# Kernel tuning notes

Hardware: AMD Instinct MI355X
Metric: run time of the kernel (lower is better)

## Reference

```python
import jax, jax.numpy as jnp
import numpy as np

A0, A1, A2 = 1.0, 1.0, 0.5
TEMPERATURE = 1.0

B, H, N, D = 2, 8, 1024, 64


def setup_inputs() -> dict:
    key = jax.random.key(0)
    k1, k2, k3, k4, k5 = jax.random.split(key, 5)
    q = jax.random.normal(k1, (B, H, N, D), dtype=jnp.float32)
    k = jax.random.normal(k2, (B, H, N, D), dtype=jnp.float32)
    v = jax.random.normal(k3, (B, H, N, D), dtype=jnp.float32)
    drop_noise = jax.random.normal(k4, (B, H, N, D), dtype=jnp.float32)
    rpe_matrix = jax.random.normal(k5, (2 * N - 1, D), dtype=jnp.float32)
    return {"q": q, "k": k, "v": v, "drop_noise": drop_noise, "rpe_matrix": rpe_matrix}


def reference(q, k, v, drop_noise, rpe_matrix):
    # Degree-2 Taylor approximation of softmax attention (fastmax):
    #   score_ij = a0 + a1*s_ij + a2*s_ij^2,  s_ij = q_i . k_j + q_i . rpe[i-j+n-1]
    #   o_i = sum_j score_ij * v_j / sum_j score_ij
    # Defaults: mask=False (bidirectional), dropout=0.0 (drop_noise unused),
    # normalize=False, temperature=1.0.
    b, h, n, d = q.shape
    qf = q.reshape(b * h, n, d)
    kf = (k / TEMPERATURE).reshape(b * h, n, d)
    vf = v.reshape(b * h, n, d)

    # dot-product term: (bh, n, n)
    qk = jnp.einsum('bid,bjd->bij', qf, kf)

    # RPE term: P[b,i,r] = q_i . rpe[r]; gather r = i - j + n - 1
    P = jnp.einsum('bid,rd->bir', qf, rpe_matrix)  # (bh, n, 2n-1)
    rel = jnp.arange(n)[:, None] - jnp.arange(n)[None, :] + (n - 1)  # (n, n)
    rel = jnp.broadcast_to(rel[None], (b * h, n, n))
    qk = qk + jnp.take_along_axis(P, rel, axis=2)

    s = A0 + A1 * qk + A2 * qk * qk  # Taylor kernel scores

    denom = jnp.sum(s, axis=-1, keepdims=True)  # (bh, n, 1)
    o = jnp.einsum('bij,bjd->bid', s, vf) / denom
    return o.reshape(b, h, n, d)
```

## Files before the change

kernel.cpp:

```cpp
#include <hip/hip_runtime.h>


#define NSEQ 1024
#define DH   64
#define BM   64
#define BN   64

typedef short bf16x8 __attribute__((ext_vector_type(8)));
typedef float f32x4  __attribute__((ext_vector_type(4)));

__device__ __forceinline__ unsigned short f2bf(float x) {
    unsigned u = __float_as_uint(x);
    u += 0x7fffu + ((u >> 16) & 1u);
    return (unsigned short)(u >> 16);
}
__device__ __forceinline__ float bf2f(unsigned short h) {
    return __uint_as_float(((unsigned)h) << 16);
}
__device__ __forceinline__ unsigned long long pack4(float4 x) {
    return (unsigned long long)f2bf(x.x)
         | ((unsigned long long)f2bf(x.y) << 16)
         | ((unsigned long long)f2bf(x.z) << 32)
         | ((unsigned long long)f2bf(x.w) << 48);
}

__global__ __launch_bounds__(512, 2)
void fastmax_kernel(const float* __restrict__ qg, const float* __restrict__ kg,
                    const float* __restrict__ vg, const float* __restrict__ rpe,
                    float* __restrict__ outg)
{
    __shared__ __align__(16) unsigned char ldsK[64 * 128];
    __shared__ __align__(16) unsigned char ldsR[128 * 128];
    __shared__ __align__(16) unsigned char ldsVT[64 * 136];
    __shared__ __align__(16) unsigned char ldsP[8 * 16 * 128];
    __shared__ __align__(16) unsigned char ldsS[8 * 16 * 80];

    const int tid = threadIdx.x;
    const int w   = tid >> 6;
    const int l   = tid & 63;
    const int lr  = l & 15;
    const int lg  = l >> 4;
    const int ws  = w >> 1;
    const int wj  = w & 1;

    const int bh = blockIdx.x >> 4;
    const int i0 = (blockIdx.x & 15) * BM;

    const float* qbh = qg + (size_t)bh * (NSEQ * DH);
    const float* kbh = kg + (size_t)bh * (NSEQ * DH);
    const float* vbh = vg + (size_t)bh * (NSEQ * DH);

    bf16x8 qf[2];
    {
        const float* qrow = qbh + (size_t)(i0 + ws * 16 + lr) * DH + lg * 8;
        #pragma unroll
        for (int kc = 0; kc < 2; ++kc) {
            float4 a = *reinterpret_cast<const float4*>(qrow + kc * 32);
            float4 b = *reinterpret_cast<const float4*>(qrow + kc * 32 + 4);
            bf16x8 f;
            f[0] = (short)f2bf(a.x); f[1] = (short)f2bf(a.y);
            f[2] = (short)f2bf(a.z); f[3] = (short)f2bf(a.w);
            f[4] = (short)f2bf(b.x); f[5] = (short)f2bf(b.y);
            f[6] = (short)f2bf(b.z); f[7] = (short)f2bf(b.w);
            qf[kc] = f;
        }
    }

    f32x4 oacc[4];
    #pragma unroll
    for (int dt = 0; dt < 4; ++dt) oacc[dt] = (f32x4){0.f, 0.f, 0.f, 0.f};
    float dp[4] = {0.f, 0.f, 0.f, 0.f};

    unsigned char* myP = ldsP + w * (16 * 128);
    unsigned char* myS = ldsS + w * (16 * 80);
    const int t0w = ws * 16 - wj * 32 + 32;

    for (int jt = 0; jt < NSEQ / BN; ++jt) {
        const int j0  = jt * BN;
        const int rlo = i0 - j0 + 960;

        __syncthreads();

        {
            const float4* src = reinterpret_cast<const float4*>(kbh + (size_t)j0 * DH);
            #pragma unroll
            for (int it = 0; it < 2; ++it) {
                int i = it * 512 + tid;
                float4 x = src[i];
                int row = i >> 4, colb = (i & 15) * 8;
                *reinterpret_cast<unsigned long long*>(
                    ldsK + ((row * 128 + colb) ^ ((row & 7) << 4))) = pack4(x);
            }
        }
        {
            #pragma unroll
            for (int it = 0; it < 4; ++it) {
                int i = it * 512 + tid;
                int row = i >> 4;
                int r = rlo + row; r = (r > 2 * NSEQ - 2) ? (2 * NSEQ - 2) : r;
                float4 x = reinterpret_cast<const float4*>(rpe + (size_t)r * DH)[i & 15];
                int colb = (i & 15) * 8;
                *reinterpret_cast<unsigned long long*>(
                    ldsR + ((row * 128 + colb) ^ ((row & 7) << 4))) = pack4(x);
            }
        }
        {
            const float4* src = reinterpret_cast<const float4*>(vbh + (size_t)j0 * DH);
            #pragma unroll
            for (int it = 0; it < 2; ++it) {
                int i = it * 512 + tid;
                float4 x = src[i];
                int j = i >> 4, d0 = (i & 15) * 4;
                unsigned char* p = ldsVT + j * 2;
                *reinterpret_cast<unsigned short*>(p + (d0 + 0) * 136) = f2bf(x.x);
                *reinterpret_cast<unsigned short*>(p + (d0 + 1) * 136) = f2bf(x.y);
                *reinterpret_cast<unsigned short*>(p + (d0 + 2) * 136) = f2bf(x.z);
                *reinterpret_cast<unsigned short*>(p + (d0 + 3) * 136) = f2bf(x.w);
            }
        }
        __syncthreads();

        f32x4 pacc[3];
        #pragma unroll
        for (int ct = 0; ct < 3; ++ct) pacc[ct] = (f32x4){0.f, 0.f, 0.f, 0.f};
        #pragma unroll
        for (int kc = 0; kc < 2; ++kc) {
            #pragma unroll
            for (int ct = 0; ct < 3; ++ct) {
                int row = t0w + ct * 16 + lr;
                bf16x8 bfrag = *reinterpret_cast<const bf16x8*>(
                    ldsR + ((row * 128 + kc * 64 + lg * 16) ^ ((row & 7) << 4)));
                pacc[ct] = __builtin_amdgcn_mfma_f32_16x16x32_bf16(qf[kc], bfrag, pacc[ct], 0, 0, 0);
            }
        }
        #pragma unroll
        for (int ct = 0; ct < 3; ++ct) {
            #pragma unroll
            for (int r = 0; r < 4; ++r) {
                int row = lg * 4 + r;
                int tl  = ct * 16 + lr;
                *reinterpret_cast<unsigned short*>(
                    myP + ((row * 128 + tl * 2) ^ ((row & 7) << 4))) = f2bf(pacc[ct][r]);
            }
        }

        f32x4 sacc[2];
        #pragma unroll
        for (int ct = 0; ct < 2; ++ct) sacc[ct] = (f32x4){0.f, 0.f, 0.f, 0.f};
        #pragma unroll
        for (int kc = 0; kc < 2; ++kc) {
            #pragma unroll
            for (int ct = 0; ct < 2; ++ct) {
                int row = wj * 32 + ct * 16 + lr;
                bf16x8 bfrag = *reinterpret_cast<const bf16x8*>(
                    ldsK + ((row * 128 + kc * 64 + lg * 16) ^ ((row & 7) << 4)));
                sacc[ct] = __builtin_amdgcn_mfma_f32_16x16x32_bf16(qf[kc], bfrag, sacc[ct], 0, 0, 0);
            }
        }

        #pragma unroll
        for (int ct = 0; ct < 2; ++ct) {
            #pragma unroll
            for (int r = 0; r < 4; ++r) {
                int row = lg * 4 + r;
                int tl  = row - ct * 16 - lr + 31;
                float pval = bf2f(*reinterpret_cast<const unsigned short*>(
                    myP + ((row * 128 + tl * 2) ^ ((row & 7) << 4))));
                float s  = sacc[ct][r] + pval;
                float sc = fmaf(s, fmaf(0.5f, s, 1.0f), 1.0f);
                dp[r] += sc;
                int jjl = ct * 16 + lr;
                *reinterpret_cast<unsigned short*>(myS + row * 80 + jjl * 2) = f2bf(sc);
            }
        }

        bf16x8 af = *reinterpret_cast<const bf16x8*>(myS + lr * 80 + lg * 16);
        #pragma unroll
        for (int dt = 0; dt < 4; ++dt) {
            const unsigned char* vp = ldsVT + (dt * 16 + lr) * 136 + wj * 64 + lg * 16;
            union { unsigned long long u[2]; bf16x8 v; } bb;
            bb.u[0] = *reinterpret_cast<const unsigned long long*>(vp);
            bb.u[1] = *reinterpret_cast<const unsigned long long*>(vp + 8);
            oacc[dt] = __builtin_amdgcn_mfma_f32_16x16x32_bf16(af, bb.v, oacc[dt], 0, 0, 0);
        }
    }

    #pragma unroll
    for (int r = 0; r < 4; ++r) {
        #pragma unroll
        for (int m = 1; m < 16; m <<= 1) dp[r] += __shfl_xor(dp[r], m, 64);
    }

    __syncthreads();
    float* ored = reinterpret_cast<float*>(ldsR);
    float* dred = reinterpret_cast<float*>(ldsK);
    if (wj == 1) {
        #pragma unroll
        for (int dt = 0; dt < 4; ++dt) {
            #pragma unroll
            for (int r = 0; r < 4; ++r) {
                int row = lg * 4 + r;
                ored[ws * 1024 + row * 64 + dt * 16 + lr] = oacc[dt][r];
            }
        }
        if (lr == 0) {
            #pragma unroll
            for (int r = 0; r < 4; ++r) dred[ws * 16 + lg * 4 + r] = dp[r];
        }
    }
    __syncthreads();
    if (wj == 0) {
        float* ob = outg + (size_t)bh * (NSEQ * DH) + (size_t)(i0 + ws * 16) * DH;
        float rd[4];
        #pragma unroll
        for (int r = 0; r < 4; ++r) {
            int row = lg * 4 + r;
            rd[r] = 1.0f / (dp[r] + dred[ws * 16 + row]);
        }
        #pragma unroll
        for (int dt = 0; dt < 4; ++dt) {
            #pragma unroll
            for (int r = 0; r < 4; ++r) {
                int row = lg * 4 + r;
                float num = oacc[dt][r] + ored[ws * 1024 + row * 64 + dt * 16 + lr];
                ob[row * DH + dt * 16 + lr] = num * rd[r];
            }
        }
    }
}

extern "C" void kernel_launch(void* const* d_in, const int* in_sizes, int n_in,
                              void* d_out, int out_size, void* d_ws, size_t ws_size,
                              hipStream_t stream) {
    const float* q   = (const float*)d_in[0];
    const float* k   = (const float*)d_in[1];
    const float* v   = (const float*)d_in[2];
    const float* rpe = (const float*)d_in[4];
    float* out = (float*)d_out;

    dim3 grid(256), block(512);
    hipLaunchKernelGGL(fastmax_kernel, grid, block, 0, stream, q, k, v, rpe, out);
}
```

Measured before the change: 117.4 us.

## Split key dimension across blocks with workspace partials and a reduction kernel

Adds a JSPLIT template that partitions the key tiles across several blocks per query tile, so the grid grows from 256 to 512 or 1024 blocks. Each warp writes its unnormalized partial output and denominator to the workspace, and a separate reduce kernel sums them and normalizes. The aim is to fill more compute units than the original grid did. In exchange it writes and reads many megabytes of fp32 partials and adds a second launch. The path taken depends on the workspace size the harness provides.

```diff
diff --git a/kernel.cpp b/kernel.cpp
--- a/kernel.cpp
+++ b/kernel.cpp
@@ -5,6 +5,9 @@
 #define DH   64
 #define BM   64
 #define BN   64
+#define NBH  16
+#define ROWS_TOTAL (NBH * NSEQ)
+#define NUM_ELEMS  ((size_t)ROWS_TOTAL * DH)
 
 typedef short bf16x8 __attribute__((ext_vector_type(8)));
 typedef float f32x4  __attribute__((ext_vector_type(4)));
@@ -24,10 +27,11 @@
          | ((unsigned long long)f2bf(x.w) << 48);
 }
 
+template<int JSPLIT>
 __global__ __launch_bounds__(512, 2)
 void fastmax_kernel(const float* __restrict__ qg, const float* __restrict__ kg,
                     const float* __restrict__ vg, const float* __restrict__ rpe,
-                    float* __restrict__ outg)
+                    float* __restrict__ outg, float* __restrict__ wsbuf)
 {
     __shared__ __align__(16) unsigned char ldsK[64 * 128];
     __shared__ __align__(16) unsigned char ldsR[128 * 128];
@@ -40,11 +44,14 @@
     const int l   = tid & 63;
     const int lr  = l & 15;
     const int lg  = l >> 4;
-    const int ws  = w >> 1;
+    const int wst = w >> 1;
     const int wj  = w & 1;
 
-    const int bh = blockIdx.x >> 4;
-    const int i0 = (blockIdx.x & 15) * BM;
+    const int b  = blockIdx.x;
+    const int js = b % JSPLIT;
+    const int it = (b / JSPLIT) & 15;
+    const int bh = b / (JSPLIT * 16);
+    const int i0 = it * BM;
 
     const float* qbh = qg + (size_t)bh * (NSEQ * DH);
     const float* kbh = kg + (size_t)bh * (NSEQ * DH);
@@ -52,16 +59,16 @@
 
     bf16x8 qf[2];
     {
-        const float* qrow = qbh + (size_t)(i0 + ws * 16 + lr) * DH + lg * 8;
+        const float* qrow = qbh + (size_t)(i0 + wst * 16 + lr) * DH + lg * 8;
         #pragma unroll
         for (int kc = 0; kc < 2; ++kc) {
             float4 a = *reinterpret_cast<const float4*>(qrow + kc * 32);
-            float4 b = *reinterpret_cast<const float4*>(qrow + kc * 32 + 4);
+            float4 b4 = *reinterpret_cast<const float4*>(qrow + kc * 32 + 4);
             bf16x8 f;
             f[0] = (short)f2bf(a.x); f[1] = (short)f2bf(a.y);
             f[2] = (short)f2bf(a.z); f[3] = (short)f2bf(a.w);
-            f[4] = (short)f2bf(b.x); f[5] = (short)f2bf(b.y);
-            f[6] = (short)f2bf(b.z); f[7] = (short)f2bf(b.w);
+            f[4] = (short)f2bf(b4.x); f[5] = (short)f2bf(b4.y);
+            f[6] = (short)f2bf(b4.z); f[7] = (short)f2bf(b4.w);
             qf[kc] = f;
         }
     }
@@ -73,9 +80,10 @@
 
     unsigned char* myP = ldsP + w * (16 * 128);
     unsigned char* myS = ldsS + w * (16 * 80);
-    const int t0w = ws * 16 - wj * 32 + 32;
-
-    for (int jt = 0; jt < NSEQ / BN; ++jt) {
+    const int t0w = wst * 16 - wj * 32 + 32;
+
+    constexpr int NJT = (NSEQ / BN) / JSPLIT;
+    for (int jt = js * NJT; jt < (js + 1) * NJT; ++jt) {
         const int j0  = jt * BN;
         const int rlo = i0 - j0 + 960;
 
@@ -84,8 +92,8 @@
         {
             const float4* src = reinterpret_cast<const float4*>(kbh + (size_t)j0 * DH);
             #pragma unroll
-            for (int it = 0; it < 2; ++it) {
-                int i = it * 512 + tid;
+            for (int itr = 0; itr < 2; ++itr) {
+                int i = itr * 512 + tid;
                 float4 x = src[i];
                 int row = i >> 4, colb = (i & 15) * 8;
                 *reinterpret_cast<unsigned long long*>(
@@ -94,8 +102,8 @@
         }
         {
             #pragma unroll
-            for (int it = 0; it < 4; ++it) {
-                int i = it * 512 + tid;
+            for (int itr = 0; itr < 4; ++itr) {
+                int i = itr * 512 + tid;
                 int row = i >> 4;
                 int r = rlo + row; r = (r > 2 * NSEQ - 2) ? (2 * NSEQ - 2) : r;
                 float4 x = reinterpret_cast<const float4*>(rpe + (size_t)r * DH)[i & 15];
@@ -107,8 +115,8 @@
         {
             const float4* src = reinterpret_cast<const float4*>(vbh + (size_t)j0 * DH);
             #pragma unroll
-            for (int it = 0; it < 2; ++it) {
-                int i = it * 512 + tid;
+            for (int itr = 0; itr < 2; ++itr) {
+                int i = itr * 512 + tid;
                 float4 x = src[i];
                 int j = i >> 4, d0 = (i & 15) * 4;
                 unsigned char* p = ldsVT + j * 2;
@@ -191,42 +199,82 @@
         for (int m = 1; m < 16; m <<= 1) dp[r] += __shfl_xor(dp[r], m, 64);
     }
 
-    __syncthreads();
-    float* ored = reinterpret_cast<float*>(ldsR);
-    float* dred = reinterpret_cast<float*>(ldsK);
-    if (wj == 1) {
-        #pragma unroll
-        for (int dt = 0; dt < 4; ++dt) {
+    if constexpr (JSPLIT == 1) {
+        __syncthreads();
+        float* ored = reinterpret_cast<float*>(ldsR);
+        float* dred = reinterpret_cast<float*>(ldsK);
+        if (wj == 1) {
+            #pragma unroll
+            for (int dt = 0; dt < 4; ++dt) {
+                #pragma unroll
+                for (int r = 0; r < 4; ++r) {
+                    int row = lg * 4 + r;
+                    ored[wst * 1024 + row * 64 + dt * 16 + lr] = oacc[dt][r];
+                }
+            }
+            if (lr == 0) {
+                #pragma unroll
+                for (int r = 0; r < 4; ++r) dred[wst * 16 + lg * 4 + r] = dp[r];
+            }
+        }
+        __syncthreads();
+        if (wj == 0) {
+            float* ob = outg + (size_t)bh * (NSEQ * DH) + (size_t)(i0 + wst * 16) * DH;
+            float rd[4];
             #pragma unroll
             for (int r = 0; r < 4; ++r) {
                 int row = lg * 4 + r;
-                ored[ws * 1024 + row * 64 + dt * 16 + lr] = oacc[dt][r];
-            }
-        }
+                rd[r] = 1.0f / (dp[r] + dred[wst * 16 + row]);
+            }
+            #pragma unroll
+            for (int dt = 0; dt < 4; ++dt) {
+                #pragma unroll
+                for (int r = 0; r < 4; ++r) {
+                    int row = lg * 4 + r;
+                    float num = oacc[dt][r] + ored[wst * 1024 + row * 64 + dt * 16 + lr];
+                    ob[row * DH + dt * 16 + lr] = num * rd[r];
+                }
+            }
+        }
+    } else {
+        const int js2  = js * 2 + wj;
+        const int rowg = bh * NSEQ + i0 + wst * 16;
+        float* nw = wsbuf + (size_t)js2 * NUM_ELEMS + (size_t)rowg * DH;
+        #pragma unroll
+        for (int dt = 0; dt < 4; ++dt) {
+            #pragma unroll
+            for (int r = 0; r < 4; ++r) {
+                nw[(lg * 4 + r) * DH + dt * 16 + lr] = oacc[dt][r];
+            }
+        }
+        float* dw = wsbuf + (size_t)(2 * JSPLIT) * NUM_ELEMS + (size_t)js2 * ROWS_TOTAL + rowg;
         if (lr == 0) {
             #pragma unroll
-            for (int r = 0; r < 4; ++r) dred[ws * 16 + lg * 4 + r] = dp[r];
-        }
-    }
-    __syncthreads();
-    if (wj == 0) {
-        float* ob = outg + (size_t)bh * (NSEQ * DH) + (size_t)(i0 + ws * 16) * DH;
-        float rd[4];
-        #pragma unroll
-        for (int r = 0; r < 4; ++r) {
-            int row = lg * 4 + r;
-            rd[r] = 1.0f / (dp[r] + dred[ws * 16 + row]);
-        }
-        #pragma unroll
-        for (int dt = 0; dt < 4; ++dt) {
-            #pragma unroll
-            for (int r = 0; r < 4; ++r) {
-                int row = lg * 4 + r;
-                float num = oacc[dt][r] + ored[ws * 1024 + row * 64 + dt * 16 + lr];
-                ob[row * DH + dt * 16 + lr] = num * rd[r];
-            }
-        }
-    }
+            for (int r = 0; r < 4; ++r) dw[lg * 4 + r] = dp[r];
+        }
+    }
+}
+
+template<int NP>
+__global__ __launch_bounds__(256)
+void reduce_kernel(const float* __restrict__ wsbuf, float* __restrict__ outg)
+{
+    const size_t idx  = (size_t)blockIdx.x * 256 + threadIdx.x;
+    const size_t flat = idx * 4;
+    const int row = (int)(flat >> 6);
+    const float* dbase = wsbuf + (size_t)NP * NUM_ELEMS;
+
+    float4 acc = make_float4(0.f, 0.f, 0.f, 0.f);
+    float den = 0.f;
+    #pragma unroll
+    for (int p = 0; p < NP; ++p) {
+        float4 x = *reinterpret_cast<const float4*>(wsbuf + (size_t)p * NUM_ELEMS + flat);
+        acc.x += x.x; acc.y += x.y; acc.z += x.z; acc.w += x.w;
+        den += dbase[(size_t)p * ROWS_TOTAL + row];
+    }
+    float rdi = 1.0f / den;
+    acc.x *= rdi; acc.y *= rdi; acc.z *= rdi; acc.w *= rdi;
+    *reinterpret_cast<float4*>(outg + flat) = acc;
 }
 
 extern "C" void kernel_launch(void* const* d_in, const int* in_sizes, int n_in,
@@ -237,7 +285,23 @@
     const float* v   = (const float*)d_in[2];
     const float* rpe = (const float*)d_in[4];
     float* out = (float*)d_out;
-
-    dim3 grid(256), block(512);
-    hipLaunchKernelGGL(fastmax_kernel, grid, block, 0, stream, q, k, v, rpe, out);
-}
+    float* wsb = (float*)d_ws;
+
+    auto need = [](int jsplit) -> size_t {
+        return ((size_t)(2 * jsplit) * NUM_ELEMS + (size_t)(2 * jsplit) * ROWS_TOTAL)
+               * sizeof(float);
+    };
+
+    if (ws_size >= need(4)) {
+        hipLaunchKernelGGL((fastmax_kernel<4>), dim3(256 * 4), dim3(512), 0, stream,
+                           q, k, v, rpe, out, wsb);
+        hipLaunchKernelGGL((reduce_kernel<8>), dim3(1024), dim3(256), 0, stream, wsb, out);
+    } else if (ws_size >= need(2)) {
+        hipLaunchKernelGGL((fastmax_kernel<2>), dim3(256 * 2), dim3(512), 0, stream,
+                           q, k, v, rpe, out, wsb);
+        hipLaunchKernelGGL((reduce_kernel<4>), dim3(1024), dim3(256), 0, stream, wsb, out);
+    } else {
+        hipLaunchKernelGGL((fastmax_kernel<1>), dim3(256), dim3(512), 0, stream,
+                           q, k, v, rpe, out, wsb);
+    }
+}
```

Measured after the change: 109.3 us. -6.9%, faster.
